# Performance work log

Hardware: AMD Instinct MI355X
Metric: run time of the kernel (lower is better)

The kernel has to match this reference:

```python
import jax, jax.numpy as jnp
import numpy as np

N = 100000
E = 1600000
IN_FEATS = 512
HIDDEN = 128
NUM_CLASSES = 2


def setup_inputs() -> dict:
    key = jax.random.key(0)
    k1, k2, k3, k4, k5, k6, k7 = jax.random.split(key, 7)
    inputs = jax.random.normal(k1, (N, IN_FEATS), dtype=jnp.float32)
    src = jax.random.randint(k2, (E,), 0, N, dtype=jnp.int64)
    dst = jax.random.randint(k3, (E,), 0, N, dtype=jnp.int64)
    # Glorot-style init like DGL GraphConv
    s1 = (6.0 / (IN_FEATS + HIDDEN)) ** 0.5
    s2 = (6.0 / (HIDDEN + NUM_CLASSES)) ** 0.5
    W1 = jax.random.uniform(k4, (IN_FEATS, HIDDEN), jnp.float32, -s1, s1)
    b1 = jnp.zeros((HIDDEN,), jnp.float32)
    W2 = jax.random.uniform(k5, (HIDDEN, NUM_CLASSES), jnp.float32, -s2, s2)
    b2 = jnp.zeros((NUM_CLASSES,), jnp.float32)
    return {"inputs": inputs, "W1": W1, "b1": b1, "W2": W2, "b2": b2,
            "src": src, "dst": dst}


def _graph_conv(x, W, b, src, dst, norm_src, norm_dst):
    # DGL GraphConv, norm='both': D_dst^{-1/2} A D_src^{-1/2} X W + b
    xw = x @ W                                   # [N, out] dense GEMM first (in >= out)
    m = (xw * norm_src[:, None])[src]            # gather messages [E, out]
    agg = jax.ops.segment_sum(m, dst, num_segments=N)  # scatter-add [N, out]
    return agg * norm_dst[:, None] + b


def reference(inputs, W1, b1, W2, b2, src, dst):
    ones = jnp.ones((src.shape[0],), jnp.float32)
    out_deg = jax.ops.segment_sum(ones, src, num_segments=N)
    in_deg = jax.ops.segment_sum(ones, dst, num_segments=N)
    norm_src = jax.lax.rsqrt(jnp.maximum(out_deg, 1.0))
    norm_dst = jax.lax.rsqrt(jnp.maximum(in_deg, 1.0))

    h = _graph_conv(inputs, W1, b1, src, dst, norm_src, norm_dst)
    h = jax.nn.relu(h)
    # dropout is identity at inference (training=False)
    h = _graph_conv(h, W2, b2, src, dst, norm_src, norm_dst)
    return jax.nn.softmax(h, axis=1)
```

## Files before the change

kernel.cpp:

```cpp
#include <hip/hip_runtime.h>
#include <math.h>

#define N_NODES 100000
#define N_EDGES 1600000
#define IN_F    512
#define HID     128

#define SH      8
#define NPB     256
#define BINS    ((N_NODES + NPB - 1) / NPB)
#define CBLK    256
#define EPB     ((N_EDGES + CBLK - 1) / CBLK)

typedef __attribute__((ext_vector_type(8))) _Float16 half8;
typedef __attribute__((ext_vector_type(2))) _Float16 half2v;
typedef __attribute__((ext_vector_type(4))) float float4v;

__device__ __forceinline__ unsigned int f16_to_e4m3bits(float xs) {
    _Float16 h = (_Float16)xs;
    unsigned short b = __builtin_bit_cast(unsigned short, h);
    unsigned int mag = (unsigned int)(b & 0x7fffu);
    mag = (mag + 0x3fu + ((mag >> 7) & 1u)) >> 7;
    if (mag > 0x7eu) mag = 0x7eu;
    return (((unsigned int)b >> 8) & 0x80u) | mag;
}

__global__ __launch_bounds__(256) void prep_kernel(const float* __restrict__ W1,
                                                   _Float16* __restrict__ W1T,
                                                   int* __restrict__ sdeg) {
    int i = blockIdx.x * 256 + threadIdx.x;
    if (i < IN_F * HID) {
        int k = i >> 7, c = i & 127;
        W1T[(size_t)c * IN_F + k] = (_Float16)W1[i];
    }
    if (i < N_NODES) sdeg[i] = 0;
}

__global__ __launch_bounds__(256) void hist_kernel(const int* __restrict__ src,
                                                   const int* __restrict__ dst,
                                                   int* __restrict__ dbh,
                                                   int* __restrict__ sdeg) {
    __shared__ int hd[BINS];
    const int t = threadIdx.x, blk = blockIdx.x;
    for (int i = t; i < BINS; i += 256) hd[i] = 0;
    __syncthreads();
    const int e0 = blk * EPB, e1 = min(N_EDGES, e0 + EPB);
    for (int e = e0 + t; e < e1; e += 256) {
        atomicAdd(&hd[dst[e] >> SH], 1);
        atomicAdd(&sdeg[src[e]], 1);
    }
    __syncthreads();
    for (int i = t; i < BINS; i += 256)
        dbh[i * CBLK + blk] = hd[i];
}

__global__ __launch_bounds__(256) void binscan_kernel(int* __restrict__ dbh,
                                                      int* __restrict__ dtot) {
    __shared__ int sh[256];
    const int b = blockIdx.x, t = threadIdx.x;
    int* arr = dbh + (size_t)b * CBLK;
    int v = arr[t];
    sh[t] = v; __syncthreads();
#pragma unroll
    for (int d = 1; d < 256; d <<= 1) {
        int u = (t >= d) ? sh[t - d] : 0;
        __syncthreads();
        sh[t] += u;
        __syncthreads();
    }
    arr[t] = sh[t] - v;
    if (t == 255) dtot[b] = sh[255];
}

__global__ __launch_bounds__(512) void binbase_kernel(const int* __restrict__ dtot,
                                                      int* __restrict__ dbase,
                                                      int* __restrict__ offs) {
    __shared__ int sh[512];
    const int t = threadIdx.x;
    int v = (t < BINS) ? dtot[t] : 0;
    sh[t] = v; __syncthreads();
#pragma unroll
    for (int d = 1; d < 512; d <<= 1) {
        int u = (t >= d) ? sh[t - d] : 0;
        __syncthreads();
        sh[t] += u;
        __syncthreads();
    }
    if (t < BINS) dbase[t] = sh[t] - v;
    if (t == BINS - 1) { dbase[BINS] = sh[t]; offs[N_NODES] = sh[t]; }
}

__global__ __launch_bounds__(256) void scatter_bins_kernel(const int* __restrict__ src,
                                                           const int* __restrict__ dst,
                                                           const int* __restrict__ dbh,
                                                           const int* __restrict__ dbase,
                                                           unsigned int* __restrict__ es) {
    __shared__ int dcur[BINS];
    const int t = threadIdx.x, blk = blockIdx.x;
    for (int i = t; i < BINS; i += 256)
        dcur[i] = dbase[i] + dbh[i * CBLK + blk];
    __syncthreads();
    const int e0 = blk * EPB, e1 = min(N_EDGES, e0 + EPB);
    for (int e = e0 + t; e < e1; e += 256) {
        int d = dst[e], s = src[e];
        int p = atomicAdd(&dcur[d >> SH], 1);
        es[p] = ((unsigned int)(d & (NPB - 1)) << 24) | (unsigned int)s;
    }
}

__global__ __launch_bounds__(256) void finalize_kernel(const unsigned int* __restrict__ es,
                                                       const int* __restrict__ sdeg,
                                                       const int* __restrict__ dbase,
                                                       int* __restrict__ csr, int* __restrict__ offs,
                                                       float* __restrict__ norm_dst,
                                                       float* __restrict__ norm_src) {
    __shared__ int cnt[NPB], pos[NPB];
    const int t = threadIdx.x, b = blockIdx.x;
    const int start = dbase[b], end = dbase[b + 1];
    cnt[t] = 0; __syncthreads();
    for (int k = start + t; k < end; k += 256)
        atomicAdd(&cnt[es[k] >> 24], 1);
    __syncthreads();
    const int c = cnt[t];
    pos[t] = c; __syncthreads();
#pragma unroll
    for (int d = 1; d < 256; d <<= 1) {
        int u = (t >= d) ? pos[t - d] : 0;
        __syncthreads();
        pos[t] += u;
        __syncthreads();
    }
    const int excl = pos[t] - c;
    const int node = (b << SH) + t;
    if (node < N_NODES) {
        offs[node] = start + excl;
        norm_dst[node] = rsqrtf(fmaxf((float)c, 1.0f));
        norm_src[node] = rsqrtf(fmaxf((float)sdeg[node], 1.0f));
    }
    cnt[t] = start + excl;
    __syncthreads();
    for (int k = start + t; k < end; k += 256) {
        unsigned int v = es[k];
        int p = atomicAdd(&cnt[v >> 24], 1);
        csr[p] = (int)(v & 0x00FFFFFFu);
    }
}

#define APAD 40
__global__ __launch_bounds__(256) void gemm1_mfma_kernel(const float* __restrict__ X,
                                                         const _Float16* __restrict__ W1T,
                                                         const float* __restrict__ norm_src,
                                                         unsigned int* __restrict__ xw8) {
    __shared__ _Float16 As[2][128 * APAD];

    const int t    = threadIdx.x;
    const int wave = t >> 6;
    const int lane = t & 63;
    const int m0   = blockIdx.x * 128;
    const int quad = lane >> 4;
    const int l16  = lane & 15;

    float4v acc[2][8];
#pragma unroll
    for (int r = 0; r < 2; r++)
#pragma unroll
        for (int c = 0; c < 8; c++) acc[r][c] = (float4v)0.f;

    const int srow = t >> 1;
    const int sc16 = (t & 1) * 16;
    const int sgrow = m0 + srow;
    const bool svalid = sgrow < N_NODES;
    const float* xbase = X + (size_t)sgrow * IN_F + sc16;

    float4 va[4];
#pragma unroll
    for (int i = 0; i < 4; i++) va[i] = make_float4(0.f, 0.f, 0.f, 0.f);
    if (svalid) {
        const float4* xp = reinterpret_cast<const float4*>(xbase);
        va[0] = xp[0]; va[1] = xp[1]; va[2] = xp[2]; va[3] = xp[3];
    }
    half8 bfrag[8];
#pragma unroll
    for (int ct = 0; ct < 8; ct++)
        bfrag[ct] = *reinterpret_cast<const half8*>(&W1T[(size_t)(ct * 16 + l16) * IN_F + quad * 8]);

    {
        half8 h0, h1;
        h0[0]=(_Float16)va[0].x; h0[1]=(_Float16)va[0].y; h0[2]=(_Float16)va[0].z; h0[3]=(_Float16)va[0].w;
        h0[4]=(_Float16)va[1].x; h0[5]=(_Float16)va[1].y; h0[6]=(_Float16)va[1].z; h0[7]=(_Float16)va[1].w;
        h1[0]=(_Float16)va[2].x; h1[1]=(_Float16)va[2].y; h1[2]=(_Float16)va[2].z; h1[3]=(_Float16)va[2].w;
        h1[4]=(_Float16)va[3].x; h1[5]=(_Float16)va[3].y; h1[6]=(_Float16)va[3].z; h1[7]=(_Float16)va[3].w;
        *reinterpret_cast<half8*>(&As[0][srow * APAD + sc16 + 0]) = h0;
        *reinterpret_cast<half8*>(&As[0][srow * APAD + sc16 + 8]) = h1;
    }

    int cur = 0;
    for (int it = 0; it < IN_F / 32; it++) {
        const int ktn = (it + 1) * 32;
        const bool more = ktn < IN_F;
        __syncthreads();

        float4 vb[4];
        half8 bnext[8];
        if (more) {
            if (svalid) {
                const float4* xp = reinterpret_cast<const float4*>(xbase + ktn);
                vb[0] = xp[0]; vb[1] = xp[1]; vb[2] = xp[2]; vb[3] = xp[3];
            } else {
                vb[0] = vb[1] = vb[2] = vb[3] = make_float4(0.f, 0.f, 0.f, 0.f);
            }
#pragma unroll
            for (int ct = 0; ct < 8; ct++)
                bnext[ct] = *reinterpret_cast<const half8*>(
                    &W1T[(size_t)(ct * 16 + l16) * IN_F + ktn + quad * 8]);
        }

        half8 afrag[2];
#pragma unroll
        for (int r = 0; r < 2; r++)
            afrag[r] = *reinterpret_cast<const half8*>(
                &As[cur][(wave * 32 + r * 16 + l16) * APAD + quad * 8]);
#pragma unroll
        for (int r = 0; r < 2; r++)
#pragma unroll
            for (int ct = 0; ct < 8; ct++)
                acc[r][ct] = __builtin_amdgcn_mfma_f32_16x16x32_f16(afrag[r], bfrag[ct], acc[r][ct], 0, 0, 0);

        if (more) {
            half8 h0, h1;
            h0[0]=(_Float16)vb[0].x; h0[1]=(_Float16)vb[0].y; h0[2]=(_Float16)vb[0].z; h0[3]=(_Float16)vb[0].w;
            h0[4]=(_Float16)vb[1].x; h0[5]=(_Float16)vb[1].y; h0[6]=(_Float16)vb[1].z; h0[7]=(_Float16)vb[1].w;
            h1[0]=(_Float16)vb[2].x; h1[1]=(_Float16)vb[2].y; h1[2]=(_Float16)vb[2].z; h1[3]=(_Float16)vb[2].w;
            h1[4]=(_Float16)vb[3].x; h1[5]=(_Float16)vb[3].y; h1[6]=(_Float16)vb[3].z; h1[7]=(_Float16)vb[3].w;
            *reinterpret_cast<half8*>(&As[cur ^ 1][srow * APAD + sc16 + 0]) = h0;
            *reinterpret_cast<half8*>(&As[cur ^ 1][srow * APAD + sc16 + 8]) = h1;
#pragma unroll
            for (int ct = 0; ct < 8; ct++) bfrag[ct] = bnext[ct];
        }
        cur ^= 1;
    }

#pragma unroll
    for (int r = 0; r < 2; r++) {
#pragma unroll
        for (int i = 0; i < 4; i++) {
            int grow = m0 + wave * 32 + r * 16 + quad * 4 + i;
            if (grow < N_NODES) {
                const float ss = norm_src[grow] * 0.00390625f;
                unsigned int by[8];
#pragma unroll
                for (int ct = 0; ct < 8; ct++) {
                    float xs = acc[r][ct][i] * ss;
                    xs = fminf(fmaxf(xs, -1.75f), 1.75f);
                    by[ct] = f16_to_e4m3bits(xs);
                }
                unsigned int w0 = by[0] | (by[1] << 8) | (by[2] << 16) | (by[3] << 24);
                unsigned int w1 = by[4] | (by[5] << 8) | (by[6] << 16) | (by[7] << 24);
                *reinterpret_cast<uint2*>(&xw8[(size_t)grow * 32 + l16 * 2]) = make_uint2(w0, w1);
            }
        }
    }
}

__global__ __launch_bounds__(256) void gather1_kernel(
        const int* __restrict__ csr, const int* __restrict__ offs,
        const unsigned int* __restrict__ xw8, const float* __restrict__ norm_dst,
        const float* __restrict__ norm_src, const float* __restrict__ b1,
        const float* __restrict__ W2, float* __restrict__ hw2) {
    const int gw   = (blockIdx.x * blockDim.x + threadIdx.x) >> 6;
    const int lane = threadIdx.x & 63;
    const int sub  = lane >> 4;
    const int l16  = lane & 15;
    const int n    = gw * 4 + sub;
    if (n >= N_NODES) return;
    const int off = offs[n], end = offs[n + 1];
    const uint2* xp = reinterpret_cast<const uint2*>(xw8);

    half2v accA = (half2v)0, accB = (half2v)0, accC = (half2v)0, accD = (half2v)0;

#define DECADD(u, aE, aO)                                                          \
    {                                                                              \
        unsigned int _u = (u);                                                     \
        unsigned int _e = ((_u & 0x00800080u) << 8) | ((_u & 0x007f007fu) << 7);   \
        unsigned int _s = _u >> 8;                                                 \
        unsigned int _o = ((_s & 0x00800080u) << 8) | ((_s & 0x007f007fu) << 7);   \
        aE += __builtin_bit_cast(half2v, _e);                                      \
        aO += __builtin_bit_cast(half2v, _o);                                      \
    }
#define ACC8(u2) { DECADD((u2).x, accA, accB) DECADD((u2).y, accC, accD) }

    int k = off;
    for (; k + 8 <= end; k += 8) {
        int s0 = csr[k], s1 = csr[k + 1], s2 = csr[k + 2], s3 = csr[k + 3];
        int s4 = csr[k + 4], s5 = csr[k + 5], s6 = csr[k + 6], s7 = csr[k + 7];
        uint2 u0 = xp[(size_t)s0 * 16 + l16];
        uint2 u1 = xp[(size_t)s1 * 16 + l16];
        uint2 u2 = xp[(size_t)s2 * 16 + l16];
        uint2 u3 = xp[(size_t)s3 * 16 + l16];
        uint2 u4 = xp[(size_t)s4 * 16 + l16];
        uint2 u5 = xp[(size_t)s5 * 16 + l16];
        uint2 u6 = xp[(size_t)s6 * 16 + l16];
        uint2 u7 = xp[(size_t)s7 * 16 + l16];
        ACC8(u0) ACC8(u1) ACC8(u2) ACC8(u3) ACC8(u4) ACC8(u5) ACC8(u6) ACC8(u7)
    }
    for (; k + 4 <= end; k += 4) {
        int s0 = csr[k], s1 = csr[k + 1], s2 = csr[k + 2], s3 = csr[k + 3];
        uint2 u0 = xp[(size_t)s0 * 16 + l16];
        uint2 u1 = xp[(size_t)s1 * 16 + l16];
        uint2 u2 = xp[(size_t)s2 * 16 + l16];
        uint2 u3 = xp[(size_t)s3 * 16 + l16];
        ACC8(u0) ACC8(u1) ACC8(u2) ACC8(u3)
    }
    for (; k < end; ++k) {
        uint2 u = xp[(size_t)csr[k] * 16 + l16];
        ACC8(u)
    }
#undef ACC8
#undef DECADD

    float a[8];
    a[0] = (float)accA[0]; a[2] = (float)accA[1];
    a[1] = (float)accB[0]; a[3] = (float)accB[1];
    a[4] = (float)accC[0]; a[6] = (float)accC[1];
    a[5] = (float)accD[0]; a[7] = (float)accD[1];

    const float nd = norm_dst[n] * 256.0f;
    float p0 = 0.f, p1 = 0.f;
#pragma unroll
    for (int ct = 0; ct < 8; ct++) {
        const int col = ct * 16 + l16;
        float h = fmaxf(a[ct] * nd + b1[col], 0.f);
        float2 w2v = reinterpret_cast<const float2*>(W2)[col];
        p0 += h * w2v.x;
        p1 += h * w2v.y;
    }
#pragma unroll
    for (int d = 1; d < 16; d <<= 1) {
        p0 += __shfl_xor(p0, d);
        p1 += __shfl_xor(p1, d);
    }
    if (l16 == 0) {
        float ns = norm_src[n];
        reinterpret_cast<float2*>(hw2)[n] = make_float2(p0 * ns, p1 * ns);
    }
}

__global__ void gather2_softmax_kernel(
        const int* __restrict__ csr, const int* __restrict__ offs,
        const float* __restrict__ hw2, const float* __restrict__ norm_dst,
        const float* __restrict__ b2, float* __restrict__ out) {
    const int w    = (blockIdx.x * blockDim.x + threadIdx.x) >> 6;
    const int lane = threadIdx.x & 63;
    const int sub  = lane >> 4, k0 = lane & 15;
    const int n = w * 4 + sub;
    if (n >= N_NODES) return;
    const int off = offs[n], end = offs[n + 1];

    float a0 = 0.f, a1 = 0.f;
    for (int k = off + k0; k < end; k += 16) {
        int s = csr[k];
        float2 v = reinterpret_cast<const float2*>(hw2)[s];
        a0 += v.x; a1 += v.y;
    }
#pragma unroll
    for (int d = 1; d < 16; d <<= 1) {
        a0 += __shfl_xor(a0, d);
        a1 += __shfl_xor(a1, d);
    }
    if (k0 == 0) {
        float nd = norm_dst[n];
        float z0 = a0 * nd + b2[0];
        float z1 = a1 * nd + b2[1];
        float m = fmaxf(z0, z1);
        float e0 = expf(z0 - m), e1 = expf(z1 - m);
        float inv = 1.f / (e0 + e1);
        reinterpret_cast<float2*>(out)[n] = make_float2(e0 * inv, e1 * inv);
    }
}

extern "C" void kernel_launch(void* const* d_in, const int* in_sizes, int n_in,
                              void* d_out, int out_size, void* d_ws, size_t ws_size,
                              hipStream_t stream) {
    const float* X   = (const float*)d_in[0];
    const float* W1  = (const float*)d_in[1];
    const float* b1  = (const float*)d_in[2];
    const float* W2  = (const float*)d_in[3];
    const float* b2  = (const float*)d_in[4];
    const int*   src = (const int*)d_in[5];
    const int*   dst = (const int*)d_in[6];
    float* out = (float*)d_out;

    const size_t N = N_NODES;
    char* ws = (char*)d_ws;
    auto alloc = [&](size_t bytes) -> char* {
        char* p = ws;
        ws += (bytes + 15) & ~(size_t)15;
        return p;
    };
    int*          dbh      = (int*)alloc((size_t)BINS * CBLK * 4);
    int*          dtot     = (int*)alloc(BINS * 4);
    int*          dbase    = (int*)alloc((BINS + 1) * 4);
    int*          sdeg     = (int*)alloc(N * 4);
    unsigned int* es       = (unsigned int*)alloc((size_t)N_EDGES * 4);
    int*          csr      = (int*)alloc((size_t)N_EDGES * 4);
    int*          offs     = (int*)alloc((N + 1) * 4);
    float*        norm_src = (float*)alloc(N * 4);
    float*        norm_dst = (float*)alloc(N * 4);
    float*        hw2      = (float*)alloc(N * 2 * 4);
    _Float16*     W1T      = (_Float16*)alloc((size_t)IN_F * HID * 2);
    unsigned int* xw8      = (unsigned int*)alloc(N * (size_t)HID);

    prep_kernel<<<(N_NODES + 255) / 256, 256, 0, stream>>>(W1, W1T, sdeg);
    hist_kernel<<<CBLK, 256, 0, stream>>>(src, dst, dbh, sdeg);
    binscan_kernel<<<BINS, 256, 0, stream>>>(dbh, dtot);
    binbase_kernel<<<1, 512, 0, stream>>>(dtot, dbase, offs);
    scatter_bins_kernel<<<CBLK, 256, 0, stream>>>(src, dst, dbh, dbase, es);
    finalize_kernel<<<BINS, 256, 0, stream>>>(es, sdeg, dbase,
                                              csr, offs, norm_dst, norm_src);
    gemm1_mfma_kernel<<<(N_NODES + 127) / 128, 256, 0, stream>>>(X, W1T, norm_src, xw8);
    gather1_kernel<<<(((N_NODES + 3) / 4) * 64 + 255) / 256, 256, 0, stream>>>(
        csr, offs, xw8, norm_dst, norm_src, b1, W2, hw2);
    gather2_softmax_kernel<<<(((int)N + 3) / 4 * 64 + 255) / 256, 256, 0, stream>>>(
        csr, offs, hw2, norm_dst, b2, out);
}
```

Baseline: 492.0 us.

## Load GEMM1 A fragments directly from global, dropping LDS staging and barriers

The first-layer GEMM no longer stages X tiles through a double-buffered LDS array with a block barrier per K step. Each wave now loads its own 16-row A fragment straight from global memory into registers, converts it to fp16, and prefetches two K steps ahead, with B fragments prefetched one step ahead. Each wave handles 16 rows instead of 32, so blocks cover 64 rows and twice as many blocks are launched. This removes LDS traffic and synchronisation, but each wave re-reads all of W1T for half as many rows, which doubles W1T fetches. The X loads are also less coalesced, since each lane fetches 32 bytes from a different row.

```diff
diff --git a/kernel.cpp b/kernel.cpp
--- a/kernel.cpp
+++ b/kernel.cpp
@@ -146,118 +146,79 @@
     }
 }
 
-#define APAD 40
 __global__ __launch_bounds__(256) void gemm1_mfma_kernel(const float* __restrict__ X,
                                                          const _Float16* __restrict__ W1T,
                                                          const float* __restrict__ norm_src,
                                                          unsigned int* __restrict__ xw8) {
-    __shared__ _Float16 As[2][128 * APAD];
-
     const int t    = threadIdx.x;
     const int wave = t >> 6;
     const int lane = t & 63;
-    const int m0   = blockIdx.x * 128;
     const int quad = lane >> 4;
     const int l16  = lane & 15;
-
-    float4v acc[2][8];
-#pragma unroll
-    for (int r = 0; r < 2; r++)
-#pragma unroll
-        for (int c = 0; c < 8; c++) acc[r][c] = (float4v)0.f;
-
-    const int srow = t >> 1;
-    const int sc16 = (t & 1) * 16;
-    const int sgrow = m0 + srow;
-    const bool svalid = sgrow < N_NODES;
-    const float* xbase = X + (size_t)sgrow * IN_F + sc16;
-
-    float4 va[4];
-#pragma unroll
-    for (int i = 0; i < 4; i++) va[i] = make_float4(0.f, 0.f, 0.f, 0.f);
-    if (svalid) {
-        const float4* xp = reinterpret_cast<const float4*>(xbase);
-        va[0] = xp[0]; va[1] = xp[1]; va[2] = xp[2]; va[3] = xp[3];
-    }
-    half8 bfrag[8];
-#pragma unroll
-    for (int ct = 0; ct < 8; ct++)
-        bfrag[ct] = *reinterpret_cast<const half8*>(&W1T[(size_t)(ct * 16 + l16) * IN_F + quad * 8]);
-
+    const int wrow = blockIdx.x * 64 + wave * 16;
+    const int arow = wrow + l16;
+    const int crow = (arow < N_NODES) ? arow : 0;
+    const float*    xa = X   + (size_t)crow * IN_F + quad * 8;
+    const _Float16* wb = W1T + (size_t)l16  * IN_F + quad * 8;
+
+    float4v acc[8];
+#pragma unroll
+    for (int c = 0; c < 8; c++) acc[c] = (float4v)0.f;
+
+    float4 A[2][2];
+    half8  B[8];
     {
-        half8 h0, h1;
-        h0[0]=(_Float16)va[0].x; h0[1]=(_Float16)va[0].y; h0[2]=(_Float16)va[0].z; h0[3]=(_Float16)va[0].w;
-        h0[4]=(_Float16)va[1].x; h0[5]=(_Float16)va[1].y; h0[6]=(_Float16)va[1].z; h0[7]=(_Float16)va[1].w;
-        h1[0]=(_Float16)va[2].x; h1[1]=(_Float16)va[2].y; h1[2]=(_Float16)va[2].z; h1[3]=(_Float16)va[2].w;
-        h1[4]=(_Float16)va[3].x; h1[5]=(_Float16)va[3].y; h1[6]=(_Float16)va[3].z; h1[7]=(_Float16)va[3].w;
-        *reinterpret_cast<half8*>(&As[0][srow * APAD + sc16 + 0]) = h0;
-        *reinterpret_cast<half8*>(&As[0][srow * APAD + sc16 + 8]) = h1;
-    }
-
-    int cur = 0;
-    for (int it = 0; it < IN_F / 32; it++) {
-        const int ktn = (it + 1) * 32;
-        const bool more = ktn < IN_F;
-        __syncthreads();
-
-        float4 vb[4];
-        half8 bnext[8];
-        if (more) {
-            if (svalid) {
-                const float4* xp = reinterpret_cast<const float4*>(xbase + ktn);
-                vb[0] = xp[0]; vb[1] = xp[1]; vb[2] = xp[2]; vb[3] = xp[3];
-            } else {
-                vb[0] = vb[1] = vb[2] = vb[3] = make_float4(0.f, 0.f, 0.f, 0.f);
+        const float4* p0 = reinterpret_cast<const float4*>(xa);
+        A[0][0] = p0[0]; A[0][1] = p0[1];
+        const float4* p1 = reinterpret_cast<const float4*>(xa + 32);
+        A[1][0] = p1[0]; A[1][1] = p1[1];
+#pragma unroll
+        for (int ct = 0; ct < 8; ct++)
+            B[ct] = *reinterpret_cast<const half8*>(wb + (size_t)(ct * 16) * IN_F);
+    }
+
+#pragma unroll
+    for (int it = 0; it < 16; ++it) {
+        const int cur = it & 1;
+        half8 fa;
+        fa[0] = (_Float16)A[cur][0].x; fa[1] = (_Float16)A[cur][0].y;
+        fa[2] = (_Float16)A[cur][0].z; fa[3] = (_Float16)A[cur][0].w;
+        fa[4] = (_Float16)A[cur][1].x; fa[5] = (_Float16)A[cur][1].y;
+        fa[6] = (_Float16)A[cur][1].z; fa[7] = (_Float16)A[cur][1].w;
+        if (it + 2 < 16) {
+            const float4* p = reinterpret_cast<const float4*>(xa + (it + 2) * 32);
+            A[cur][0] = p[0]; A[cur][1] = p[1];
+        }
+        half8 Bc[8];
+#pragma unroll
+        for (int ct = 0; ct < 8; ct++) Bc[ct] = B[ct];
+        if (it + 1 < 16) {
+#pragma unroll
+            for (int ct = 0; ct < 8; ct++)
+                B[ct] = *reinterpret_cast<const half8*>(
+                    wb + (size_t)(ct * 16) * IN_F + (it + 1) * 32);
+        }
+#pragma unroll
+        for (int ct = 0; ct < 8; ct++)
+            acc[ct] = __builtin_amdgcn_mfma_f32_16x16x32_f16(fa, Bc[ct], acc[ct], 0, 0, 0);
+    }
+
+    const int grow = wrow + quad * 4;
+#pragma unroll
+    for (int i = 0; i < 4; i++) {
+        const int g = grow + i;
+        if (g < N_NODES) {
+            const float ss = norm_src[g] * 0.00390625f;
+            unsigned int by[8];
+#pragma unroll
+            for (int ct = 0; ct < 8; ct++) {
+                float xs = acc[ct][i] * ss;
+                xs = fminf(fmaxf(xs, -1.75f), 1.75f);
+                by[ct] = f16_to_e4m3bits(xs);
             }
-#pragma unroll
-            for (int ct = 0; ct < 8; ct++)
-                bnext[ct] = *reinterpret_cast<const half8*>(
-                    &W1T[(size_t)(ct * 16 + l16) * IN_F + ktn + quad * 8]);
-        }
-
-        half8 afrag[2];
-#pragma unroll
-        for (int r = 0; r < 2; r++)
-            afrag[r] = *reinterpret_cast<const half8*>(
-                &As[cur][(wave * 32 + r * 16 + l16) * APAD + quad * 8]);
-#pragma unroll
-        for (int r = 0; r < 2; r++)
-#pragma unroll
-            for (int ct = 0; ct < 8; ct++)
-                acc[r][ct] = __builtin_amdgcn_mfma_f32_16x16x32_f16(afrag[r], bfrag[ct], acc[r][ct], 0, 0, 0);
-
-        if (more) {
-            half8 h0, h1;
-            h0[0]=(_Float16)vb[0].x; h0[1]=(_Float16)vb[0].y; h0[2]=(_Float16)vb[0].z; h0[3]=(_Float16)vb[0].w;
-            h0[4]=(_Float16)vb[1].x; h0[5]=(_Float16)vb[1].y; h0[6]=(_Float16)vb[1].z; h0[7]=(_Float16)vb[1].w;
-            h1[0]=(_Float16)vb[2].x; h1[1]=(_Float16)vb[2].y; h1[2]=(_Float16)vb[2].z; h1[3]=(_Float16)vb[2].w;
-            h1[4]=(_Float16)vb[3].x; h1[5]=(_Float16)vb[3].y; h1[6]=(_Float16)vb[3].z; h1[7]=(_Float16)vb[3].w;
-            *reinterpret_cast<half8*>(&As[cur ^ 1][srow * APAD + sc16 + 0]) = h0;
-            *reinterpret_cast<half8*>(&As[cur ^ 1][srow * APAD + sc16 + 8]) = h1;
-#pragma unroll
-            for (int ct = 0; ct < 8; ct++) bfrag[ct] = bnext[ct];
-        }
-        cur ^= 1;
-    }
-
-#pragma unroll
-    for (int r = 0; r < 2; r++) {
-#pragma unroll
-        for (int i = 0; i < 4; i++) {
-            int grow = m0 + wave * 32 + r * 16 + quad * 4 + i;
-            if (grow < N_NODES) {
-                const float ss = norm_src[grow] * 0.00390625f;
-                unsigned int by[8];
-#pragma unroll
-                for (int ct = 0; ct < 8; ct++) {
-                    float xs = acc[r][ct][i] * ss;
-                    xs = fminf(fmaxf(xs, -1.75f), 1.75f);
-                    by[ct] = f16_to_e4m3bits(xs);
-                }
-                unsigned int w0 = by[0] | (by[1] << 8) | (by[2] << 16) | (by[3] << 24);
-                unsigned int w1 = by[4] | (by[5] << 8) | (by[6] << 16) | (by[7] << 24);
-                *reinterpret_cast<uint2*>(&xw8[(size_t)grow * 32 + l16 * 2]) = make_uint2(w0, w1);
-            }
+            unsigned int w0 = by[0] | (by[1] << 8) | (by[2] << 16) | (by[3] << 24);
+            unsigned int w1 = by[4] | (by[5] << 8) | (by[6] << 16) | (by[7] << 24);
+            *reinterpret_cast<uint2*>(&xw8[(size_t)g * 32 + l16 * 2]) = make_uint2(w0, w1);
         }
     }
 }
@@ -417,7 +378,7 @@
     scatter_bins_kernel<<<CBLK, 256, 0, stream>>>(src, dst, dbh, dbase, es);
     finalize_kernel<<<BINS, 256, 0, stream>>>(es, sdeg, dbase,
                                               csr, offs, norm_dst, norm_src);
-    gemm1_mfma_kernel<<<(N_NODES + 127) / 128, 256, 0, stream>>>(X, W1T, norm_src, xw8);
+    gemm1_mfma_kernel<<<(N_NODES + 63) / 64, 256, 0, stream>>>(X, W1T, norm_src, xw8);
     gather1_kernel<<<(((N_NODES + 3) / 4) * 64 + 255) / 256, 256, 0, stream>>>(
         csr, offs, xw8, norm_dst, norm_src, b1, W2, hw2);
     gather2_softmax_kernel<<<(((int)N + 3) / 4 * 64 + 255) / 256, 256, 0, stream>>>(
```

After: 557.6 us. 1.13x slower.
